# Kernel optimization log

Hardware: AMD Instinct MI355X
Metric: run time of the kernel (lower is better)

The kernel has to match this reference:

```python
import jax, jax.numpy as jnp
import numpy as np

B, S, D, H = 2, 2048, 1024, 16
DK = D // H


def setup_inputs() -> dict:
    key = jax.random.key(0)
    ks = jax.random.split(key, 8)
    scale = 1.0 / np.sqrt(D)
    inp = {
        "query": jax.random.normal(ks[0], (B, S, D), dtype=jnp.float32),
        "key": jax.random.normal(ks[1], (B, S, D), dtype=jnp.float32),
        "value": jax.random.normal(ks[2], (B, S, D), dtype=jnp.float32),
        # causal mask, broadcastable over batch and heads
        "mask": jnp.tril(jnp.ones((S, S), dtype=jnp.int32))[None, None, :, :],
        "W_q": jax.random.normal(ks[3], (D, D), dtype=jnp.float32) * scale,
        "W_k": jax.random.normal(ks[4], (D, D), dtype=jnp.float32) * scale,
        "W_v": jax.random.normal(ks[5], (D, D), dtype=jnp.float32) * scale,
        "W_o": jax.random.normal(ks[6], (D, D), dtype=jnp.float32) * scale,
    }
    return inp


def _split_heads(t):
    Bb, Ss, _ = t.shape
    return t.reshape(Bb, Ss, H, DK).transpose(0, 2, 1, 3)  # [B,H,S,DK]


def reference(query, key, value, mask, W_q, W_k, W_v, W_o):
    # Linear(d,d,bias=False): y = x @ W^T (torch stores weight as [out,in])
    Q = _split_heads(query @ W_q.T)
    K = _split_heads(key @ W_k.T)
    V = _split_heads(value @ W_v.T)
    scores = jnp.einsum("bhqd,bhkd->bhqk", Q, K) / jnp.sqrt(jnp.float32(DK))
    scores = jnp.where(mask == 0, -jnp.inf, scores)
    weights = jax.nn.softmax(scores, axis=-1)
    weights = jnp.nan_to_num(weights, nan=0.0)  # fully-masked rows -> 0
    # dropout is identity at inference
    x = jnp.einsum("bhqk,bhkd->bhqd", weights, V)
    x = x.transpose(0, 2, 1, 3).reshape(B, S, D)
    return x @ W_o.T
```

## Files before the change

### kernel.cpp

```cpp
#include <hip/hip_runtime.h>
#include <hip/hip_bf16.h>

#define D_MODEL 1024
#define NHEAD   16
#define HDK     64
#define SEQ     2048
#define BATCH   2
#define BS      (BATCH * SEQ)

typedef __attribute__((ext_vector_type(8))) short bf16x8;
typedef __attribute__((ext_vector_type(4))) float f32x4;
typedef __attribute__((ext_vector_type(4))) unsigned int u32x4;

__device__ __forceinline__ unsigned short f2bf(float f) {
    unsigned u = __builtin_bit_cast(unsigned, f);
    u += 0x7fffu + ((u >> 16) & 1u);
    return (unsigned short)(u >> 16);
}

__device__ __forceinline__ unsigned pack_hi(float x, float y) {
    return __builtin_amdgcn_perm(__builtin_bit_cast(unsigned, y),
                                 __builtin_bit_cast(unsigned, x), 0x07060302u);
}

__device__ __forceinline__ float exp2_fast(float x) {
    float r;
    asm("v_exp_f32 %0, %1" : "=v"(r) : "v"(x));
    return r;
}

__device__ __forceinline__ float max3(float a, float b, float c) {
    return fmaxf(fmaxf(a, b), c);
}

typedef const void __attribute__((address_space(1))) gas_void;
typedef void __attribute__((address_space(3))) las_void;

__device__ __forceinline__ void gll16(const void* g, void* l) {
    __builtin_amdgcn_global_load_lds((gas_void*)g, (las_void*)l, 16, 0, 0);
}

__device__ __forceinline__ void cast_body(const float* __restrict__ src,
                                          unsigned short* __restrict__ dst, int i) {
    const float4* p = (const float4*)src + (size_t)i * 2;
    float4 a = p[0], b = p[1];
    ushort4 lo = make_ushort4(f2bf(a.x), f2bf(a.y), f2bf(a.z), f2bf(a.w));
    ushort4 hi = make_ushort4(f2bf(b.x), f2bf(b.y), f2bf(b.z), f2bf(b.w));
    ushort4* q = (ushort4*)dst + (size_t)i * 2;
    q[0] = lo; q[1] = hi;
}

__global__ __launch_bounds__(256)
void cast_act(const float* a, const float* b, const float* c,
              unsigned short* oa, unsigned short* ob, unsigned short* oc, int n8) {
    int i = blockIdx.x * 256 + threadIdx.x;
    if (i >= n8) return;
    const float* s = blockIdx.y == 0 ? a : blockIdx.y == 1 ? b : c;
    unsigned short* d = blockIdx.y == 0 ? oa : blockIdx.y == 1 ? ob : oc;
    cast_body(s, d, i);
}

__global__ __launch_bounds__(256)
void cast_wt(const float* a, const float* b, const float* c, const float* dd,
             unsigned short* oa, unsigned short* ob, unsigned short* oc, unsigned short* od, int n8) {
    int i = blockIdx.x * 256 + threadIdx.x;
    if (i >= n8) return;
    const float* s = blockIdx.y == 0 ? a : blockIdx.y == 1 ? b : blockIdx.y == 2 ? c : dd;
    unsigned short* d = blockIdx.y == 0 ? oa : blockIdx.y == 1 ? ob : blockIdx.y == 2 ? oc : od;
    cast_body(s, d, i);
}

__device__ __forceinline__ void gemm_kloop128(const unsigned short* __restrict__ X,
                                              const unsigned short* __restrict__ W,
                                              unsigned short* As, unsigned short* Bs,
                                              int bm, int bn, f32x4 acc[4][4]) {
    const int t    = threadIdx.x;
    const int w    = t >> 6;
    const int L    = t & 63;
    const int quad = L >> 4;
    const int lm   = L & 15;
    const int r8   = L >> 3;
    const int sl   = L & 7;
    const int xcol = ((sl ^ r8) & 7) * 8;
    const int wr   = (w >> 1) * 64;
    const int wc   = (w & 1) * 64;

    for (int kt = 0; kt < D_MODEL; kt += 64) {
        __syncthreads();
        #pragma unroll
        for (int i = 0; i < 4; ++i) {
            int c = w * 4 + i;
            gll16(X + (size_t)(bm + c * 8 + r8) * D_MODEL + kt + xcol, &As[c * 512]);
        }
        #pragma unroll
        for (int i = 0; i < 4; ++i) {
            int c = w * 4 + i;
            gll16(W + (size_t)(bn + c * 8 + r8) * D_MODEL + kt + xcol, &Bs[c * 512]);
        }
        __syncthreads();

        #pragma unroll
        for (int ch = 0; ch < 2; ++ch) {
            bf16x8 af[4], bfr[4];
            #pragma unroll
            for (int ms = 0; ms < 4; ++ms) {
                int row = wr + ms * 16 + lm;
                af[ms] = *(const bf16x8*)&As[row * 64 + (((ch * 4 + quad) ^ (row & 7)) * 8)];
            }
            #pragma unroll
            for (int ns = 0; ns < 4; ++ns) {
                int row = wc + ns * 16 + lm;
                bfr[ns] = *(const bf16x8*)&Bs[row * 64 + (((ch * 4 + quad) ^ (row & 7)) * 8)];
            }
            #pragma unroll
            for (int ms = 0; ms < 4; ++ms)
                #pragma unroll
                for (int ns = 0; ns < 4; ++ns)
                    acc[ms][ns] = __builtin_amdgcn_mfma_f32_16x16x32_bf16(
                        af[ms], bfr[ns], acc[ms][ns], 0, 0, 0);
        }
    }
}

__device__ __forceinline__ void gemm_kloop64(const unsigned short* __restrict__ X,
                                             const unsigned short* __restrict__ W,
                                             unsigned short* As, unsigned short* Bs,
                                             int bm, int bn, f32x4 acc[2][4]) {
    const int t    = threadIdx.x;
    const int w    = t >> 6;
    const int L    = t & 63;
    const int quad = L >> 4;
    const int lm   = L & 15;
    const int r8   = L >> 3;
    const int sl   = L & 7;
    const int xcol = ((sl ^ r8) & 7) * 8;

    for (int kt = 0; kt < D_MODEL; kt += 64) {
        __syncthreads();
        #pragma unroll
        for (int i = 0; i < 4; ++i) {
            int c = w * 4 + i;
            gll16(X + (size_t)(bm + c * 8 + r8) * D_MODEL + kt + xcol, &As[c * 512]);
        }
        #pragma unroll
        for (int i = 0; i < 2; ++i) {
            int c = w * 2 + i;
            gll16(W + (size_t)(bn + c * 8 + r8) * D_MODEL + kt + xcol, &Bs[c * 512]);
        }
        __syncthreads();

        #pragma unroll
        for (int ch = 0; ch < 2; ++ch) {
            bf16x8 af[2], bfr[4];
            #pragma unroll
            for (int ms = 0; ms < 2; ++ms) {
                int row = w * 32 + ms * 16 + lm;
                af[ms] = *(const bf16x8*)&As[row * 64 + (((ch * 4 + quad) ^ (row & 7)) * 8)];
            }
            #pragma unroll
            for (int ns = 0; ns < 4; ++ns) {
                int row = ns * 16 + lm;
                bfr[ns] = *(const bf16x8*)&Bs[row * 64 + (((ch * 4 + quad) ^ (row & 7)) * 8)];
            }
            #pragma unroll
            for (int ms = 0; ms < 2; ++ms)
                #pragma unroll
                for (int ns = 0; ns < 4; ++ns)
                    acc[ms][ns] = __builtin_amdgcn_mfma_f32_16x16x32_bf16(
                        af[ms], bfr[ns], acc[ms][ns], 0, 0, 0);
        }
    }
}

__global__ __launch_bounds__(256, 3)
void proj_gemm(const unsigned short* __restrict__ qx, const unsigned short* __restrict__ kx,
               const unsigned short* __restrict__ vx, const unsigned short* __restrict__ wq,
               const unsigned short* __restrict__ wk, const unsigned short* __restrict__ wv,
               unsigned short* __restrict__ Qp, unsigned short* __restrict__ Kp,
               unsigned short* __restrict__ VT) {
    __shared__ __align__(16) unsigned short As[128 * 64];
    __shared__ __align__(16) unsigned short Bs[128 * 64];

    const int p = blockIdx.z;
    const unsigned short* X = p == 0 ? qx : p == 1 ? kx : vx;
    const unsigned short* W = p == 0 ? wq : p == 1 ? wk : wv;
    const int bm = blockIdx.y * 128, bn = blockIdx.x * 128;

    f32x4 acc[4][4];
    #pragma unroll
    for (int ms = 0; ms < 4; ++ms)
        #pragma unroll
        for (int ns = 0; ns < 4; ++ns)
            acc[ms][ns] = (f32x4){0.f, 0.f, 0.f, 0.f};

    gemm_kloop128(X, W, As, Bs, bm, bn, acc);

    const int t = threadIdx.x, w = t >> 6, L = t & 63, quad = L >> 4, lm = L & 15;
    const int wr = (w >> 1) * 64, wc = (w & 1) * 64;
    if (p == 2) {
        const int b    = bm >> 11;
        const int s_in = (bm & (SEQ - 1)) + wr;
        #pragma unroll
        for (int ms = 0; ms < 4; ++ms)
            #pragma unroll
            for (int ns = 0; ns < 4; ++ns) {
                int dg = bn + wc + ns * 16 + lm;
                int h  = dg >> 6, d = dg & 63;
                ushort4 pk = make_ushort4(f2bf(acc[ms][ns][0]), f2bf(acc[ms][ns][1]),
                                          f2bf(acc[ms][ns][2]), f2bf(acc[ms][ns][3]));
                *(ushort4*)&VT[((size_t)((b * NHEAD + h) * HDK + d)) * SEQ +
                               s_in + ms * 16 + quad * 4] = pk;
            }
    } else {
        unsigned short* Y = p == 0 ? Qp : Kp;
        const float scl = p == 0 ? 0.18033688011112042f : 1.0f;
        #pragma unroll
        for (int ms = 0; ms < 4; ++ms)
            #pragma unroll
            for (int ns = 0; ns < 4; ++ns)
                #pragma unroll
                for (int r = 0; r < 4; ++r)
                    Y[(size_t)(bm + wr + ms * 16 + quad * 4 + r) * D_MODEL +
                      bn + wc + ns * 16 + lm] = f2bf(acc[ms][ns][r] * scl);
    }
}

__global__ __launch_bounds__(256)
void out_gemm(const unsigned short* __restrict__ X, const unsigned short* __restrict__ W,
              float* __restrict__ Y) {
    __shared__ __align__(16) unsigned short As[128 * 64];
    __shared__ __align__(16) unsigned short Bs[64 * 64];
    const int bm = blockIdx.y * 128, bn = blockIdx.x * 64;

    f32x4 acc[2][4];
    #pragma unroll
    for (int ms = 0; ms < 2; ++ms)
        #pragma unroll
        for (int ns = 0; ns < 4; ++ns)
            acc[ms][ns] = (f32x4){0.f, 0.f, 0.f, 0.f};

    gemm_kloop64(X, W, As, Bs, bm, bn, acc);

    const int t = threadIdx.x, w = t >> 6, L = t & 63, quad = L >> 4, lm = L & 15;
    #pragma unroll
    for (int ms = 0; ms < 2; ++ms)
        #pragma unroll
        for (int ns = 0; ns < 4; ++ns)
            #pragma unroll
            for (int r = 0; r < 4; ++r)
                Y[(size_t)(bm + w * 32 + ms * 16 + quad * 4 + r) * D_MODEL +
                  bn + ns * 16 + lm] = acc[ms][ns][r];
}

__global__ __launch_bounds__(256, 4)
void attn_mfma(const unsigned short* __restrict__ Q, const unsigned short* __restrict__ K,
               const unsigned short* __restrict__ VT, unsigned short* __restrict__ A,
               float* __restrict__ PO, float* __restrict__ PML) {
    __shared__ __align__(16) unsigned short Ks[2][64 * 64];
    __shared__ __align__(16) unsigned short Vs[2][64 * 64];

    const int t    = threadIdx.x;
    const int w    = t >> 6;
    const int L    = t & 63;
    const int quad = L >> 4;
    const int lm   = L & 15;
    const int r8   = L >> 3;
    const int sl   = L & 7;
    const int xcol = (sl ^ r8) * 8;

    const int id = blockIdx.x;
    int qt, bh, k_lo, k_hi, slot;
    if (id < 1024) {
        qt = 31 - (id >> 6);
        const int j    = id & 63;
        const int half = j >> 5;
        bh = j & 31;
        const int c = (qt + 2) >> 1;
        k_lo = half ? c : 0;
        k_hi = half ? qt + 1 : c;
        slot = ((qt - 16) * 32 + bh) * 2 + half;
    } else {
        const int j = id - 1024;
        qt = 15 - (j >> 5);
        bh = j & 31;
        k_lo = 0; k_hi = qt + 1;
        slot = -1;
    }
    const int h = bh & 15;
    const int b = bh >> 4;

    const size_t hb   = (size_t)b * SEQ * D_MODEL + h * HDK;
    const size_t vrow = (size_t)(b * NHEAD + h) * HDK * SEQ;

    const unsigned short* kbase = K + hb;
    const unsigned short* vbase = VT + vrow;

    const int q0   = qt * 64;
    const int qrow = q0 + w * 16 + lm;

    auto stage = [&](int k0, int buf) {
        #pragma unroll
        for (int i = 0; i < 2; ++i) {
            int row = (w * 2 + i) * 8 + r8;
            gll16(kbase + (size_t)(k0 + row) * D_MODEL + xcol, &Ks[buf][(w * 2 + i) * 512]);
            gll16(vbase + (size_t)row * SEQ + k0 + xcol,       &Vs[buf][(w * 2 + i) * 512]);
        }
    };

    stage(k_lo * 64, 0);

    bf16x8 Qf0, Qf1;
    {
        const unsigned short* qp = Q + hb + (size_t)qrow * D_MODEL + quad * 8;
        Qf0 = *(const bf16x8*)qp;
        Qf1 = *(const bf16x8*)(qp + 32);
    }

    f32x4 Oacc[4];
    #pragma unroll
    for (int nt = 0; nt < 4; ++nt) Oacc[nt] = (f32x4){0.f, 0.f, 0.f, 0.f};
    float m_run  = -INFINITY;
    float l_lane = 0.f;

    __syncthreads();

    int bb = 0;
    for (int kt = k_lo; kt < k_hi; ++kt) {
        const int k0 = kt * 64;
        const unsigned short* Kc = Ks[bb];
        const unsigned short* Vc = Vs[bb];
        if (kt + 1 < k_hi) stage((kt + 1) * 64, bb ^ 1);

        f32x4 S[4];
        __builtin_amdgcn_s_setprio(1);
        #pragma unroll
        for (int ct = 0; ct < 4; ++ct) {
            bf16x8 a0 = *(const bf16x8*)&Kc[(ct * 16 + lm) * 64 + ((quad ^ (lm & 7)) * 8)];
            bf16x8 a1 = *(const bf16x8*)&Kc[(ct * 16 + lm) * 64 + (((4 + quad) ^ (lm & 7)) * 8)];
            f32x4 z = (f32x4){0.f, 0.f, 0.f, 0.f};
            z = __builtin_amdgcn_mfma_f32_16x16x32_bf16(a0, Qf0, z, 0, 0, 0);
            z = __builtin_amdgcn_mfma_f32_16x16x32_bf16(a1, Qf1, z, 0, 0, 0);
            S[ct] = z;
        }
        __builtin_amdgcn_s_setprio(0);

        if (k0 + 63 > q0 + w * 16) {
            #pragma unroll
            for (int ct = 0; ct < 4; ++ct)
                #pragma unroll
                for (int r = 0; r < 4; ++r)
                    if ((k0 + ct * 16 + quad * 4 + r) > qrow)
                        S[ct][r] = -1e30f;
        }

        float ma = max3(S[0][0], S[0][1], S[0][2]);
        float mb = max3(S[0][3], S[1][0], S[1][1]);
        float mc = max3(S[1][2], S[1][3], S[2][0]);
        float md = max3(S[2][1], S[2][2], S[2][3]);
        float me = max3(S[3][0], S[3][1], S[3][2]);
        float ml = max3(max3(ma, mb, mc), md, me);
        ml = fmaxf(ml, S[3][3]);
        if (__any(ml > m_run + 8.0f)) {
            float m = fmaxf(ml, __shfl_xor(ml, 16));
            m = fmaxf(m, __shfl_xor(m, 32));
            const float m_new = fmaxf(m_run, m);
            const float alpha = exp2_fast(m_run - m_new);
            #pragma unroll
            for (int nt = 0; nt < 4; ++nt)
                #pragma unroll
                for (int r = 0; r < 4; ++r) Oacc[nt][r] *= alpha;
            l_lane *= alpha;
            m_run = m_new;
        }
        #pragma unroll
        for (int ct = 0; ct < 4; ++ct)
            #pragma unroll
            for (int r = 0; r < 4; ++r)
                S[ct][r] = exp2_fast(S[ct][r] - m_run);
        {
            float p0 = (S[0][0] + S[0][1]) + (S[0][2] + S[0][3]);
            float p1 = (S[1][0] + S[1][1]) + (S[1][2] + S[1][3]);
            float p2 = (S[2][0] + S[2][1]) + (S[2][2] + S[2][3]);
            float p3 = (S[3][0] + S[3][1]) + (S[3][2] + S[3][3]);
            l_lane += (p0 + p1) + (p2 + p3);
        }

        unsigned x0 = pack_hi(S[0][0], S[0][1]);
        unsigned x1 = pack_hi(S[0][2], S[0][3]);
        unsigned y0 = pack_hi(S[1][0], S[1][1]);
        unsigned y1 = pack_hi(S[1][2], S[1][3]);
        asm("v_permlane32_swap_b32 %0, %1" : "+v"(x0), "+v"(y0));
        asm("v_permlane32_swap_b32 %0, %1" : "+v"(x1), "+v"(y1));
        asm("v_permlane16_swap_b32 %0, %1" : "+v"(x0), "+v"(y0));
        asm("v_permlane16_swap_b32 %0, %1" : "+v"(x1), "+v"(y1));
        bf16x8 Pb0 = __builtin_bit_cast(bf16x8, (u32x4){x0, x1, y0, y1});
        unsigned x2 = pack_hi(S[2][0], S[2][1]);
        unsigned x3 = pack_hi(S[2][2], S[2][3]);
        unsigned y2 = pack_hi(S[3][0], S[3][1]);
        unsigned y3 = pack_hi(S[3][2], S[3][3]);
        asm("v_permlane32_swap_b32 %0, %1" : "+v"(x2), "+v"(y2));
        asm("v_permlane32_swap_b32 %0, %1" : "+v"(x3), "+v"(y3));
        asm("v_permlane16_swap_b32 %0, %1" : "+v"(x2), "+v"(y2));
        asm("v_permlane16_swap_b32 %0, %1" : "+v"(x3), "+v"(y3));
        bf16x8 Pb1 = __builtin_bit_cast(bf16x8, (u32x4){x2, x3, y2, y3});

        __builtin_amdgcn_s_setprio(1);
        #pragma unroll
        for (int nt = 0; nt < 4; ++nt) {
            bf16x8 a0 = *(const bf16x8*)&Vc[(nt * 16 + lm) * 64 + ((quad ^ (lm & 7)) * 8)];
            bf16x8 a1 = *(const bf16x8*)&Vc[(nt * 16 + lm) * 64 + (((4 + quad) ^ (lm & 7)) * 8)];
            f32x4 o = Oacc[nt];
            o = __builtin_amdgcn_mfma_f32_16x16x32_bf16(a0, Pb0, o, 0, 0, 0);
            o = __builtin_amdgcn_mfma_f32_16x16x32_bf16(a1, Pb1, o, 0, 0, 0);
            Oacc[nt] = o;
        }
        __builtin_amdgcn_s_setprio(0);

        __syncthreads();
        bb ^= 1;
    }

    float l_row = l_lane + __shfl_xor(l_lane, 16);
    l_row += __shfl_xor(l_row, 32);

    if (slot >= 0) {
        float4* po = (float4*)(PO + (size_t)slot * 4096);
        #pragma unroll
        for (int nt = 0; nt < 4; ++nt)
            po[t * 4 + nt] = __builtin_bit_cast(float4, Oacc[nt]);
        if (quad == 0) {
            PML[slot * 128 + w * 16 + lm]      = m_run;
            PML[slot * 128 + 64 + w * 16 + lm] = l_row;
        }
    } else {
        const float inv_l = 1.f / l_row;
        unsigned short* es = &Ks[0][w * 1024];
        #pragma unroll
        for (int nt = 0; nt < 4; ++nt) {
            ushort4 pk = make_ushort4(f2bf(Oacc[nt][0] * inv_l), f2bf(Oacc[nt][1] * inv_l),
                                      f2bf(Oacc[nt][2] * inv_l), f2bf(Oacc[nt][3] * inv_l));
            int lc = 2 * nt + (quad >> 1);
            *(ushort4*)&es[lm * 64 + ((lc ^ (lm & 7)) * 8) + (quad & 1) * 4] = pk;
        }
        #pragma unroll
        for (int pp = 0; pp < 2; ++pp) {
            int qr = pp * 8 + r8;
            int dc = sl * 8;
            uint4 val = *(const uint4*)&es[qr * 64 + ((sl ^ (qr & 7)) * 8)];
            *(uint4*)&A[hb + (size_t)(q0 + w * 16 + qr) * D_MODEL + dc] = val;
        }
    }
}

__global__ __launch_bounds__(256)
void attn_combine(const float* __restrict__ PO, const float* __restrict__ PML,
                  unsigned short* __restrict__ A) {
    __shared__ __align__(16) unsigned short es_[4][16 * 64];

    const int t    = threadIdx.x;
    const int w    = t >> 6;
    const int L    = t & 63;
    const int quad = L >> 4;
    const int lm   = L & 15;
    const int r8   = L >> 3;
    const int sl   = L & 7;

    const int r  = blockIdx.x;
    const int qt = 16 + (r >> 5);
    const int bh = r & 31;
    const int h  = bh & 15;
    const int b  = bh >> 4;
    const size_t hb = (size_t)b * SEQ * D_MODEL + h * HDK;
    const int q0 = qt * 64;
    const int q  = w * 16 + lm;

    const float* ml1 = PML + (size_t)(r * 2 + 0) * 128;
    const float* ml2 = PML + (size_t)(r * 2 + 1) * 128;
    const float m1 = ml1[q], l1 = ml1[64 + q];
    const float m2 = ml2[q], l2 = ml2[64 + q];
    const float M  = fmaxf(m1, m2);
    const float e1 = exp2_fast(m1 - M);
    const float e2 = exp2_fast(m2 - M);
    const float inv = 1.f / (e1 * l1 + e2 * l2);
    const float c1 = e1 * inv, c2 = e2 * inv;

    const float4* o1 = (const float4*)(PO + (size_t)(r * 2 + 0) * 4096);
    const float4* o2 = (const float4*)(PO + (size_t)(r * 2 + 1) * 4096);

    unsigned short* es = &es_[w][0];
    #pragma unroll
    for (int nt = 0; nt < 4; ++nt) {
        float4 a = o1[t * 4 + nt];
        float4 c = o2[t * 4 + nt];
        float v0 = a.x * c1 + c.x * c2;
        float v1 = a.y * c1 + c.y * c2;
        float v2 = a.z * c1 + c.z * c2;
        float v3 = a.w * c1 + c.w * c2;
        ushort4 pk = make_ushort4(f2bf(v0), f2bf(v1), f2bf(v2), f2bf(v3));
        int lc = 2 * nt + (quad >> 1);
        *(ushort4*)&es[lm * 64 + ((lc ^ (lm & 7)) * 8) + (quad & 1) * 4] = pk;
    }
    #pragma unroll
    for (int pp = 0; pp < 2; ++pp) {
        int qr = pp * 8 + r8;
        int dc = sl * 8;
        uint4 val = *(const uint4*)&es[qr * 64 + ((sl ^ (qr & 7)) * 8)];
        *(uint4*)&A[hb + (size_t)(q0 + w * 16 + qr) * D_MODEL + dc] = val;
    }
}

extern "C" void kernel_launch(void* const* d_in, const int* in_sizes, int n_in,
                              void* d_out, int out_size, void* d_ws, size_t ws_size,
                              hipStream_t stream) {
    const float* q  = (const float*)d_in[0];
    const float* k  = (const float*)d_in[1];
    const float* v  = (const float*)d_in[2];
    const float* Wq = (const float*)d_in[4];
    const float* Wk = (const float*)d_in[5];
    const float* Wv = (const float*)d_in[6];
    const float* Wo = (const float*)d_in[7];
    float* out = (float*)d_out;

    char* ws = (char*)d_ws;
    const size_t MB = 1024 * 1024;
    unsigned short* qb  = (unsigned short*)(ws + 0 * MB);
    unsigned short* kb  = (unsigned short*)(ws + 8 * MB);
    unsigned short* vb  = (unsigned short*)(ws + 16 * MB);
    unsigned short* wqb = (unsigned short*)(ws + 24 * MB);
    unsigned short* wkb = (unsigned short*)(ws + 26 * MB);
    unsigned short* wvb = (unsigned short*)(ws + 28 * MB);
    unsigned short* wob = (unsigned short*)(ws + 30 * MB);
    unsigned short* Qp  = (unsigned short*)(ws + 32 * MB);
    unsigned short* Kp  = (unsigned short*)(ws + 40 * MB);
    unsigned short* VTp = (unsigned short*)(ws + 48 * MB);
    unsigned short* Ap  = (unsigned short*)(ws + 56 * MB);
    float* PO  = (float*)(ws + 0 * MB);
    float* PML = (float*)(ws + 16 * MB);

    const int nX8 = BS * D_MODEL / 8;
    const int nW8 = D_MODEL * D_MODEL / 8;
    cast_act<<<dim3(nX8 / 256, 3), 256, 0, stream>>>(q, k, v, qb, kb, vb, nX8);
    cast_wt <<<dim3(nW8 / 256, 4), 256, 0, stream>>>(Wq, Wk, Wv, Wo, wqb, wkb, wvb, wob, nW8);

    proj_gemm<<<dim3(D_MODEL / 128, BS / 128, 3), 256, 0, stream>>>(
        qb, kb, vb, wqb, wkb, wvb, Qp, Kp, VTp);

    attn_mfma<<<dim3(1536), 256, 0, stream>>>(Qp, Kp, VTp, Ap, PO, PML);
    attn_combine<<<dim3(512), 256, 0, stream>>>(PO, PML, Ap);

    out_gemm<<<dim3(D_MODEL / 64, BS / 128), 256, 0, stream>>>(Ap, wob, out);
}
```

Measured before the change: 216.9 us.

## Register-staged K/V prefetch in attention, merge cast kernels, add combine barrier

The attention loop stops using direct global-to-LDS loads and instead loads the next K/V tile into registers two tiles ahead, writing it to LDS one step ahead. A lighter barrier waits only on LDS counters, and the loop is unrolled by two so buffer indices are compile-time constants. The two cast launches are merged into one kernel to save a launch. A missing __syncthreads is added in the combine kernel between the LDS writes and the LDS reads of other threads. The cost is more registers and an extra LDS write pass per tile.

New measurement: 221.1 us. No clear change (+1.9%).

```diff
diff --git a/kernel.cpp b/kernel.cpp
--- a/kernel.cpp
+++ b/kernel.cpp
@@ -38,6 +38,12 @@
 
 __device__ __forceinline__ void gll16(const void* g, void* l) {
     __builtin_amdgcn_global_load_lds((gas_void*)g, (las_void*)l, 16, 0, 0);
+}
+
+__device__ __forceinline__ void tile_barrier() {
+    asm volatile("s_waitcnt lgkmcnt(0)" ::: "memory");
+    __builtin_amdgcn_sched_barrier(0);
+    __builtin_amdgcn_s_barrier();
 }
 
 __device__ __forceinline__ void cast_body(const float* __restrict__ src,
@@ -51,22 +57,27 @@
 }
 
 __global__ __launch_bounds__(256)
-void cast_act(const float* a, const float* b, const float* c,
-              unsigned short* oa, unsigned short* ob, unsigned short* oc, int n8) {
-    int i = blockIdx.x * 256 + threadIdx.x;
-    if (i >= n8) return;
-    const float* s = blockIdx.y == 0 ? a : blockIdx.y == 1 ? b : c;
-    unsigned short* d = blockIdx.y == 0 ? oa : blockIdx.y == 1 ? ob : oc;
-    cast_body(s, d, i);
-}
-
-__global__ __launch_bounds__(256)
-void cast_wt(const float* a, const float* b, const float* c, const float* dd,
-             unsigned short* oa, unsigned short* ob, unsigned short* oc, unsigned short* od, int n8) {
-    int i = blockIdx.x * 256 + threadIdx.x;
-    if (i >= n8) return;
-    const float* s = blockIdx.y == 0 ? a : blockIdx.y == 1 ? b : blockIdx.y == 2 ? c : dd;
-    unsigned short* d = blockIdx.y == 0 ? oa : blockIdx.y == 1 ? ob : blockIdx.y == 2 ? oc : od;
+void cast_all(const float* x0, const float* x1, const float* x2,
+              const float* w0, const float* w1, const float* w2, const float* w3,
+              unsigned short* y0, unsigned short* y1, unsigned short* y2,
+              unsigned short* z0, unsigned short* z1, unsigned short* z2,
+              unsigned short* z3) {
+    const int id = blockIdx.x;
+    const float* s;
+    unsigned short* d;
+    int i;
+    if (id < 6144) {
+        const int which = id >> 11;
+        i = (id & 2047) * 256 + threadIdx.x;
+        s = which == 0 ? x0 : which == 1 ? x1 : x2;
+        d = which == 0 ? y0 : which == 1 ? y1 : y2;
+    } else {
+        const int j = id - 6144;
+        const int which = j >> 9;
+        i = (j & 511) * 256 + threadIdx.x;
+        s = which == 0 ? w0 : which == 1 ? w1 : which == 2 ? w2 : w3;
+        d = which == 0 ? z0 : which == 1 ? z1 : which == 2 ? z2 : z3;
+    }
     cast_body(s, d, i);
 }
 
@@ -298,16 +309,22 @@
     const int q0   = qt * 64;
     const int qrow = q0 + w * 16 + lm;
 
-    auto stage = [&](int k0, int buf) {
-        #pragma unroll
-        for (int i = 0; i < 2; ++i) {
-            int row = (w * 2 + i) * 8 + r8;
-            gll16(kbase + (size_t)(k0 + row) * D_MODEL + xcol, &Ks[buf][(w * 2 + i) * 512]);
-            gll16(vbase + (size_t)row * SEQ + k0 + xcol,       &Vs[buf][(w * 2 + i) * 512]);
-        }
+    const int row0 = (w * 2 + 0) * 8 + r8;
+    const int row1 = (w * 2 + 1) * 8 + r8;
+
+    float4 kr0, kr1, vr0, vr1;
+    auto issue_loads = [&](int k0) {
+        kr0 = *(const float4*)(kbase + (size_t)(k0 + row0) * D_MODEL + xcol);
+        kr1 = *(const float4*)(kbase + (size_t)(k0 + row1) * D_MODEL + xcol);
+        vr0 = *(const float4*)(vbase + (size_t)row0 * SEQ + k0 + xcol);
+        vr1 = *(const float4*)(vbase + (size_t)row1 * SEQ + k0 + xcol);
     };
-
-    stage(k_lo * 64, 0);
+    auto write_lds = [&](int buf) {
+        *(float4*)&Ks[buf][(w * 2 + 0) * 512 + L * 8] = kr0;
+        *(float4*)&Ks[buf][(w * 2 + 1) * 512 + L * 8] = kr1;
+        *(float4*)&Vs[buf][(w * 2 + 0) * 512 + L * 8] = vr0;
+        *(float4*)&Vs[buf][(w * 2 + 1) * 512 + L * 8] = vr1;
+    };
 
     bf16x8 Qf0, Qf1;
     {
@@ -322,21 +339,24 @@
     float m_run  = -INFINITY;
     float l_lane = 0.f;
 
-    __syncthreads();
-
-    int bb = 0;
-    for (int kt = k_lo; kt < k_hi; ++kt) {
+    issue_loads(k_lo * 64);
+    write_lds(0);
+    if (k_lo + 1 < k_hi) issue_loads((k_lo + 1) * 64);
+    tile_barrier();
+
+    auto tile_step = [&](int kt, int buf) {
         const int k0 = kt * 64;
-        const unsigned short* Kc = Ks[bb];
-        const unsigned short* Vc = Vs[bb];
-        if (kt + 1 < k_hi) stage((kt + 1) * 64, bb ^ 1);
+        if (kt + 1 < k_hi) {
+            write_lds(buf ^ 1);
+            if (kt + 2 < k_hi) issue_loads((kt + 2) * 64);
+        }
 
         f32x4 S[4];
         __builtin_amdgcn_s_setprio(1);
         #pragma unroll
         for (int ct = 0; ct < 4; ++ct) {
-            bf16x8 a0 = *(const bf16x8*)&Kc[(ct * 16 + lm) * 64 + ((quad ^ (lm & 7)) * 8)];
-            bf16x8 a1 = *(const bf16x8*)&Kc[(ct * 16 + lm) * 64 + (((4 + quad) ^ (lm & 7)) * 8)];
+            bf16x8 a0 = *(const bf16x8*)&Ks[buf][(ct * 16 + lm) * 64 + ((quad ^ (lm & 7)) * 8)];
+            bf16x8 a1 = *(const bf16x8*)&Ks[buf][(ct * 16 + lm) * 64 + (((4 + quad) ^ (lm & 7)) * 8)];
             f32x4 z = (f32x4){0.f, 0.f, 0.f, 0.f};
             z = __builtin_amdgcn_mfma_f32_16x16x32_bf16(a0, Qf0, z, 0, 0, 0);
             z = __builtin_amdgcn_mfma_f32_16x16x32_bf16(a1, Qf1, z, 0, 0, 0);
@@ -407,8 +427,8 @@
         __builtin_amdgcn_s_setprio(1);
         #pragma unroll
         for (int nt = 0; nt < 4; ++nt) {
-            bf16x8 a0 = *(const bf16x8*)&Vc[(nt * 16 + lm) * 64 + ((quad ^ (lm & 7)) * 8)];
-            bf16x8 a1 = *(const bf16x8*)&Vc[(nt * 16 + lm) * 64 + (((4 + quad) ^ (lm & 7)) * 8)];
+            bf16x8 a0 = *(const bf16x8*)&Vs[buf][(nt * 16 + lm) * 64 + ((quad ^ (lm & 7)) * 8)];
+            bf16x8 a1 = *(const bf16x8*)&Vs[buf][(nt * 16 + lm) * 64 + (((4 + quad) ^ (lm & 7)) * 8)];
             f32x4 o = Oacc[nt];
             o = __builtin_amdgcn_mfma_f32_16x16x32_bf16(a0, Pb0, o, 0, 0, 0);
             o = __builtin_amdgcn_mfma_f32_16x16x32_bf16(a1, Pb1, o, 0, 0, 0);
@@ -416,8 +436,15 @@
         }
         __builtin_amdgcn_s_setprio(0);
 
-        __syncthreads();
-        bb ^= 1;
+        tile_barrier();
+    };
+
+    int kt = k_lo;
+    for (;;) {
+        tile_step(kt, 0);
+        if (++kt == k_hi) break;
+        tile_step(kt, 1);
+        if (++kt == k_hi) break;
     }
 
     float l_row = l_lane + __shfl_xor(l_lane, 16);
@@ -500,6 +527,7 @@
         int lc = 2 * nt + (quad >> 1);
         *(ushort4*)&es[lm * 64 + ((lc ^ (lm & 7)) * 8) + (quad & 1) * 4] = pk;
     }
+    __syncthreads();
     #pragma unroll
     for (int pp = 0; pp < 2; ++pp) {
         int qr = pp * 8 + r8;
@@ -537,10 +565,8 @@
     float* PO  = (float*)(ws + 0 * MB);
     float* PML = (float*)(ws + 16 * MB);
 
-    const int nX8 = BS * D_MODEL / 8;
-    const int nW8 = D_MODEL * D_MODEL / 8;
-    cast_act<<<dim3(nX8 / 256, 3), 256, 0, stream>>>(q, k, v, qb, kb, vb, nX8);
-    cast_wt <<<dim3(nW8 / 256, 4), 256, 0, stream>>>(Wq, Wk, Wv, Wo, wqb, wkb, wvb, wob, nW8);
+    cast_all<<<dim3(8192), 256, 0, stream>>>(q, k, v, Wq, Wk, Wv, Wo,
+                                             qb, kb, vb, wqb, wkb, wvb, wob);
 
     proj_gemm<<<dim3(D_MODEL / 128, BS / 128, 3), 256, 0, stream>>>(
         qb, kb, vb, wqb, wkb, wvb, Qp, Kp, VTp);
```

## Fuse split-KV combine into attention via atomic last-arriver and merge cast kernels

Applied to the files above, without the earlier changes.

Removes the separate attn_combine launch. Each split-KV attention block now writes its partials, fences, and increments a per-pair atomic counter. The second block of a pair to arrive merges its in-register output with the partner's stored partial and writes the bf16 result, then resets the counter. The two cast kernels are also merged into one launch. This saves two kernel launches and a re-read of the partials. In exchange it adds fences, atomics and a global flag array that relies on being zero-initialised and reset correctly between calls.

Result: slower. 415.9 us (+91.7%).

```diff
diff --git a/kernel.cpp b/kernel.cpp
--- a/kernel.cpp
+++ b/kernel.cpp
@@ -11,6 +11,8 @@
 typedef __attribute__((ext_vector_type(8))) short bf16x8;
 typedef __attribute__((ext_vector_type(4))) float f32x4;
 typedef __attribute__((ext_vector_type(4))) unsigned int u32x4;
+
+__device__ unsigned g_flags[512];
 
 __device__ __forceinline__ unsigned short f2bf(float f) {
     unsigned u = __builtin_bit_cast(unsigned, f);
@@ -51,22 +53,27 @@
 }
 
 __global__ __launch_bounds__(256)
-void cast_act(const float* a, const float* b, const float* c,
-              unsigned short* oa, unsigned short* ob, unsigned short* oc, int n8) {
-    int i = blockIdx.x * 256 + threadIdx.x;
-    if (i >= n8) return;
-    const float* s = blockIdx.y == 0 ? a : blockIdx.y == 1 ? b : c;
-    unsigned short* d = blockIdx.y == 0 ? oa : blockIdx.y == 1 ? ob : oc;
-    cast_body(s, d, i);
-}
-
-__global__ __launch_bounds__(256)
-void cast_wt(const float* a, const float* b, const float* c, const float* dd,
-             unsigned short* oa, unsigned short* ob, unsigned short* oc, unsigned short* od, int n8) {
-    int i = blockIdx.x * 256 + threadIdx.x;
-    if (i >= n8) return;
-    const float* s = blockIdx.y == 0 ? a : blockIdx.y == 1 ? b : blockIdx.y == 2 ? c : dd;
-    unsigned short* d = blockIdx.y == 0 ? oa : blockIdx.y == 1 ? ob : blockIdx.y == 2 ? oc : od;
+void cast_all(const float* x0, const float* x1, const float* x2,
+              const float* w0, const float* w1, const float* w2, const float* w3,
+              unsigned short* y0, unsigned short* y1, unsigned short* y2,
+              unsigned short* z0, unsigned short* z1, unsigned short* z2,
+              unsigned short* z3) {
+    const int id = blockIdx.x;
+    const float* s;
+    unsigned short* d;
+    int i;
+    if (id < 6144) {
+        const int which = id >> 11;
+        i = (id & 2047) * 256 + threadIdx.x;
+        s = which == 0 ? x0 : which == 1 ? x1 : x2;
+        d = which == 0 ? y0 : which == 1 ? y1 : y2;
+    } else {
+        const int j = id - 6144;
+        const int which = j >> 9;
+        i = (j & 511) * 256 + threadIdx.x;
+        s = which == 0 ? w0 : which == 1 ? w1 : which == 2 ? w2 : w3;
+        d = which == 0 ? z0 : which == 1 ? z1 : which == 2 ? z2 : z3;
+    }
     cast_body(s, d, i);
 }
 
@@ -432,6 +439,42 @@
             PML[slot * 128 + w * 16 + lm]      = m_run;
             PML[slot * 128 + 64 + w * 16 + lm] = l_row;
         }
+        __threadfence();
+        __syncthreads();
+        int* fs = (int*)&Vs[0][0];
+        if (t == 0) *fs = (int)atomicAdd(&g_flags[slot >> 1], 1u);
+        __syncthreads();
+        if (*fs == 1) {
+            __threadfence();
+            const int r2   = slot ^ 1;
+            const int q    = w * 16 + lm;
+            const float m2 = PML[r2 * 128 + q];
+            const float l2 = PML[r2 * 128 + 64 + q];
+            const float M  = fmaxf(m_run, m2);
+            const float e1 = exp2_fast(m_run - M);
+            const float e2 = exp2_fast(m2 - M);
+            const float inv = 1.f / (e1 * l_row + e2 * l2);
+            const float c1 = e1 * inv, c2 = e2 * inv;
+            const float4* po2 = (const float4*)(PO + (size_t)r2 * 4096);
+            unsigned short* es = &Ks[0][w * 1024];
+            #pragma unroll
+            for (int nt = 0; nt < 4; ++nt) {
+                float4 c = po2[t * 4 + nt];
+                ushort4 pk = make_ushort4(
+                    f2bf(Oacc[nt][0] * c1 + c.x * c2), f2bf(Oacc[nt][1] * c1 + c.y * c2),
+                    f2bf(Oacc[nt][2] * c1 + c.z * c2), f2bf(Oacc[nt][3] * c1 + c.w * c2));
+                int lc = 2 * nt + (quad >> 1);
+                *(ushort4*)&es[lm * 64 + ((lc ^ (lm & 7)) * 8) + (quad & 1) * 4] = pk;
+            }
+            #pragma unroll
+            for (int pp = 0; pp < 2; ++pp) {
+                int qr = pp * 8 + r8;
+                int dc = sl * 8;
+                uint4 val = *(const uint4*)&es[qr * 64 + ((sl ^ (qr & 7)) * 8)];
+                *(uint4*)&A[hb + (size_t)(q0 + w * 16 + qr) * D_MODEL + dc] = val;
+            }
+            if (t == 0) atomicExch(&g_flags[slot >> 1], 0u);
+        }
     } else {
         const float inv_l = 1.f / l_row;
         unsigned short* es = &Ks[0][w * 1024];
@@ -449,63 +492,6 @@
             uint4 val = *(const uint4*)&es[qr * 64 + ((sl ^ (qr & 7)) * 8)];
             *(uint4*)&A[hb + (size_t)(q0 + w * 16 + qr) * D_MODEL + dc] = val;
         }
-    }
-}
-
-__global__ __launch_bounds__(256)
-void attn_combine(const float* __restrict__ PO, const float* __restrict__ PML,
-                  unsigned short* __restrict__ A) {
-    __shared__ __align__(16) unsigned short es_[4][16 * 64];
-
-    const int t    = threadIdx.x;
-    const int w    = t >> 6;
-    const int L    = t & 63;
-    const int quad = L >> 4;
-    const int lm   = L & 15;
-    const int r8   = L >> 3;
-    const int sl   = L & 7;
-
-    const int r  = blockIdx.x;
-    const int qt = 16 + (r >> 5);
-    const int bh = r & 31;
-    const int h  = bh & 15;
-    const int b  = bh >> 4;
-    const size_t hb = (size_t)b * SEQ * D_MODEL + h * HDK;
-    const int q0 = qt * 64;
-    const int q  = w * 16 + lm;
-
-    const float* ml1 = PML + (size_t)(r * 2 + 0) * 128;
-    const float* ml2 = PML + (size_t)(r * 2 + 1) * 128;
-    const float m1 = ml1[q], l1 = ml1[64 + q];
-    const float m2 = ml2[q], l2 = ml2[64 + q];
-    const float M  = fmaxf(m1, m2);
-    const float e1 = exp2_fast(m1 - M);
-    const float e2 = exp2_fast(m2 - M);
-    const float inv = 1.f / (e1 * l1 + e2 * l2);
-    const float c1 = e1 * inv, c2 = e2 * inv;
-
-    const float4* o1 = (const float4*)(PO + (size_t)(r * 2 + 0) * 4096);
-    const float4* o2 = (const float4*)(PO + (size_t)(r * 2 + 1) * 4096);
-
-    unsigned short* es = &es_[w][0];
-    #pragma unroll
-    for (int nt = 0; nt < 4; ++nt) {
-        float4 a = o1[t * 4 + nt];
-        float4 c = o2[t * 4 + nt];
-        float v0 = a.x * c1 + c.x * c2;
-        float v1 = a.y * c1 + c.y * c2;
-        float v2 = a.z * c1 + c.z * c2;
-        float v3 = a.w * c1 + c.w * c2;
-        ushort4 pk = make_ushort4(f2bf(v0), f2bf(v1), f2bf(v2), f2bf(v3));
-        int lc = 2 * nt + (quad >> 1);
-        *(ushort4*)&es[lm * 64 + ((lc ^ (lm & 7)) * 8) + (quad & 1) * 4] = pk;
-    }
-    #pragma unroll
-    for (int pp = 0; pp < 2; ++pp) {
-        int qr = pp * 8 + r8;
-        int dc = sl * 8;
-        uint4 val = *(const uint4*)&es[qr * 64 + ((sl ^ (qr & 7)) * 8)];
-        *(uint4*)&A[hb + (size_t)(q0 + w * 16 + qr) * D_MODEL + dc] = val;
     }
 }
 
@@ -537,16 +523,13 @@
     float* PO  = (float*)(ws + 0 * MB);
     float* PML = (float*)(ws + 16 * MB);
 
-    const int nX8 = BS * D_MODEL / 8;
-    const int nW8 = D_MODEL * D_MODEL / 8;
-    cast_act<<<dim3(nX8 / 256, 3), 256, 0, stream>>>(q, k, v, qb, kb, vb, nX8);
-    cast_wt <<<dim3(nW8 / 256, 4), 256, 0, stream>>>(Wq, Wk, Wv, Wo, wqb, wkb, wvb, wob, nW8);
+    cast_all<<<dim3(8192), 256, 0, stream>>>(q, k, v, Wq, Wk, Wv, Wo,
+                                             qb, kb, vb, wqb, wkb, wvb, wob);
 
     proj_gemm<<<dim3(D_MODEL / 128, BS / 128, 3), 256, 0, stream>>>(
         qb, kb, vb, wqb, wkb, wvb, Qp, Kp, VTp);
 
     attn_mfma<<<dim3(1536), 256, 0, stream>>>(Qp, Kp, VTp, Ap, PO, PML);
-    attn_combine<<<dim3(512), 256, 0, stream>>>(PO, PML, Ap);
 
     out_gemm<<<dim3(D_MODEL / 64, BS / 128), 256, 0, stream>>>(Ap, wob, out);
 }
```
